# Kernel optimization log

Hardware: AMD Instinct MI355X
Metric: run time of the kernel (lower is better)

## Reference

```python
import jax, jax.numpy as jnp
import numpy as np

B, NPTS, NBOX = 16, 100000, 64
PTS_THRESHOLD = 2048          # topk voxels kept per scene
GT_THRESHOLD = 2.5            # distance multiplier
VOXEL_SIZE = 0.01
TENSOR_STRIDE = 8             # stride of the level being pruned
SIZE = TENSOR_STRIDE * VOXEL_SIZE  # 0.08, per-voxel cell size at this level


def setup_inputs() -> dict:
    key = jax.random.key(0)
    k1, k2, k3 = jax.random.split(key, 3)
    scores = jax.random.normal(k1, (B, NPTS), dtype=jnp.float32)
    points = jax.random.uniform(k2, (B, NPTS, 3), dtype=jnp.float32)
    gt_centers = jax.random.uniform(k3, (B, NBOX, 3), dtype=jnp.float32)
    return {"scores": scores, "points": points, "gt_centers": gt_centers}


def reference(scores, points, gt_centers):
    # --- per-batch topk score mask (MEFPN3D._get_score_mask) ---
    _, idx = jax.lax.top_k(scores, PTS_THRESHOLD)          # [B, K]
    score_mask = jnp.zeros(scores.shape, dtype=bool)
    score_mask = score_mask.at[jnp.arange(B)[:, None], idx].set(True)  # scatter True

    # --- gt distance mask (MEFPN3D._get_gt_mask) ---
    # distances: [B, Npts, n_boxes]
    diff = points[:, :, None, :] - gt_centers[:, None, :, :]
    distances = jnp.sqrt(jnp.sum(diff * diff, axis=-1))
    gt_mask = jnp.any(distances < SIZE * GT_THRESHOLD, axis=-1)        # [B, Npts]

    # --- combined prune mask (scatter of per-batch masks into global mask) ---
    prune_mask = jnp.logical_or(score_mask, gt_mask)

    # --- per-voxel sigmoid BCE loss, reduction='none' (CrossEntropyLoss use_sigmoid=True) ---
    target = gt_mask.astype(scores.dtype)
    losses = target * jax.nn.softplus(-scores) + (1.0 - target) * jax.nn.softplus(scores)
    return prune_mask, losses
```

## Files before the change

kernel.cpp:

```cpp
#include <hip/hip_runtime.h>
#include <hip/hip_bf16.h>
#include <stdint.h>

#define BB 16
#define NPTS 100000
#define NBOX 64
#define KTOP 2048
#define THRF 0.2f
#define C_LO 0.039984f
#define C_HI 0.040016f

#define SLICES 16
#define SLICE_SPAN 6272
#define SCAP 512
#define LIST_CAP 4096
#define CUT 0xC0000000u

#define CAND_OFF 0
#define CNT_OFF  (BB * SLICES * SCAP)
#define STATE_OFF (CNT_OFF + BB * SLICES)
#define TBOX_OFF  (STATE_OFF + BB * 2)

__device__ __forceinline__ uint32_t fmap(float f) {
    uint32_t b = __float_as_uint(f);
    return (b & 0x80000000u) ? ~b : (b | 0x80000000u);
}

__global__ __launch_bounds__(256) void cand_k(const float* __restrict__ scores,
                                              uint32_t* __restrict__ ws) {
    __shared__ uint32_t buf[SCAP];
    __shared__ uint32_t lcnt;
    const int b = blockIdx.y, sl = blockIdx.x, tid = threadIdx.x;
    if (tid == 0) lcnt = 0;
    __syncthreads();
    const int start = sl * SLICE_SPAN;
    const int nf4 = min(SLICE_SPAN, NPTS - start) >> 2;
    const float4* sc4 = reinterpret_cast<const float4*>(scores + (size_t)b * NPTS + start);
    for (int i4 = tid; i4 < nf4; i4 += 256) {
        const float4 v = sc4[i4];
        const uint32_t u[4] = {fmap(v.x), fmap(v.y), fmap(v.z), fmap(v.w)};
#pragma unroll
        for (int j = 0; j < 4; ++j) {
            if (u[j] >= CUT) {
                const uint32_t pos = atomicAdd(&lcnt, 1u);
                if (pos < SCAP) buf[pos] = u[j];
            }
        }
    }
    __syncthreads();
    const uint32_t c = lcnt;
    uint32_t* dst = ws + CAND_OFF + ((size_t)(b * SLICES + sl)) * SCAP;
    const uint32_t cw = c < SCAP ? c : SCAP;
    for (uint32_t i = tid; i < cw; i += 256) dst[i] = buf[i];
    if (tid == 0) ws[CNT_OFF + b * SLICES + sl] = c;
}

__device__ __forceinline__ void pick256(const uint32_t* __restrict__ hist,
                                        uint32_t* __restrict__ excl,
                                        int tid, int lane, uint32_t target,
                                        uint32_t* sBin, uint32_t* sKrem,
                                        uint32_t* sE, uint32_t* sTot, int wantE) {
    __syncthreads();
    if (tid < 64) {
        const uint32_t v0 = hist[4*tid], v1 = hist[4*tid+1], v2 = hist[4*tid+2], v3 = hist[4*tid+3];
        const uint32_t lt = v0 + v1 + v2 + v3;
        uint32_t x = lt;
#pragma unroll
        for (int off = 1; off < 64; off <<= 1) {
            const uint32_t y = __shfl_up(x, off);
            if (lane >= off) x += y;
        }
        const uint32_t ex = x - lt;
        excl[4*tid] = ex; excl[4*tid+1] = ex + v0;
        excl[4*tid+2] = ex + v0 + v1; excl[4*tid+3] = ex + v0 + v1 + v2;
        if (tid == 63) *sTot = x;
    }
    __syncthreads();
    {
        const uint32_t total = *sTot, lim = total - target;
        const uint32_t pe = excl[tid];
        const uint32_t pe1 = (tid == 255) ? total : excl[tid + 1];
        if (pe <= lim && pe1 > lim) {
            *sBin = (uint32_t)tid;
            *sKrem = target - (total - pe1);
            if (wantE) *sE = pe1 - pe;
        }
    }
    __syncthreads();
}

__global__ __launch_bounds__(256) void selfin_k(const float* __restrict__ scores,
                                                const float* __restrict__ ctrs,
                                                uint32_t* __restrict__ ws) {
    const int b = blockIdx.x, tid = threadIdx.x, w = tid >> 6, lane = tid & 63;
    __shared__ uint32_t list[LIST_CAP];
    __shared__ uint32_t h4[4][257];
    __shared__ uint32_t hist[256], excl[256];
    __shared__ uint32_t scnt[SLICES], soff[SLICES];
    __shared__ uint32_t wcnt[4];
    __shared__ uint32_t sBin, sKrem, sE, sTot, sIstar, sRun, sSpec, sUni, lcnt;

    const float* sc = scores + (size_t)b * NPTS;

    if (tid < NBOX) {
        const float cx = ctrs[(size_t)b * NBOX * 3 + 3 * tid];
        const float cy = ctrs[(size_t)b * NBOX * 3 + 3 * tid + 1];
        const float cz = ctrs[(size_t)b * NBOX * 3 + 3 * tid + 2];
        float4* TB = reinterpret_cast<float4*>(ws + TBOX_OFF) + b * NBOX;
        TB[tid] = make_float4(-2.0f * cx, -2.0f * cy, -2.0f * cz,
                              fmaf(cx, cx, fmaf(cy, cy, cz * cz)));
    }

    if (tid < SLICES) scnt[tid] = ws[CNT_OFF + b * SLICES + tid];
    __syncthreads();
    if (tid == 0) {
        uint32_t tot = 0; bool ok = true;
        for (int s = 0; s < SLICES; ++s) {
            soff[s] = tot;
            const uint32_t c = scnt[s];
            if (c > SCAP) ok = false;
            tot += c;
        }
        sTot = tot;
        sSpec = (ok && tot >= KTOP && tot <= LIST_CAP) ? 1u : 0u;
        sKrem = KTOP;
        sIstar = NPTS;
        lcnt = 0;
        sUni = 1u;
    }
    __syncthreads();

    uint32_t cnt, prefix = 0u;
    int shift0;
    if (sSpec) {
        cnt = sTot;
#pragma unroll 2
        for (int s = 0; s < SLICES; ++s) {
            const uint32_t c = scnt[s], o = soff[s];
            const uint32_t* src = ws + CAND_OFF + ((size_t)(b * SLICES + s)) * SCAP;
            for (uint32_t i = tid; i < c; i += 256) list[o + i] = src[i];
        }
        __syncthreads();
        const uint32_t b0 = list[0] >> 24;
        bool uni = true;
        for (uint32_t i = tid; i < cnt; i += 256) uni &= ((list[i] >> 24) == b0);
        if (!uni) atomicAnd(&sUni, 0u);
        __syncthreads();
        if (sUni) { prefix = b0 << 24; shift0 = 16; }
        else      { prefix = 0u;       shift0 = 24; }
    } else {
        for (int i = tid; i < 4 * 257; i += 256) (&h4[0][0])[i] = 0;
        __syncthreads();
        const float4* sc4 = reinterpret_cast<const float4*>(sc);
        for (int i4 = tid; i4 < NPTS / 4; i4 += 256) {
            const float4 v = sc4[i4];
            atomicAdd(&h4[w][fmap(v.x) >> 24], 1u);
            atomicAdd(&h4[w][fmap(v.y) >> 24], 1u);
            atomicAdd(&h4[w][fmap(v.z) >> 24], 1u);
            atomicAdd(&h4[w][fmap(v.w) >> 24], 1u);
        }
        __syncthreads();
        hist[tid] = h4[0][tid] + h4[1][tid] + h4[2][tid] + h4[3][tid];
        pick256(hist, excl, tid, lane, KTOP, &sBin, &sKrem, &sE, &sTot, 0);
        const uint32_t beta = sBin;
        for (int i4 = tid; i4 < NPTS / 4; i4 += 256) {
            const float4 v = sc4[i4];
            const uint32_t u[4] = {fmap(v.x), fmap(v.y), fmap(v.z), fmap(v.w)};
#pragma unroll
            for (int j = 0; j < 4; ++j) {
                if ((u[j] >> 24) == beta) {
                    const uint32_t pos = atomicAdd(&lcnt, 1u);
                    if (pos < LIST_CAP) list[pos] = u[j];
                }
            }
        }
        __syncthreads();
        cnt = lcnt < LIST_CAP ? lcnt : LIST_CAP;
        prefix = beta << 24;
        shift0 = 16;
    }

#pragma unroll 1
    for (int shift = shift0; shift >= 0; shift -= 8) {
        for (int i = tid; i < 4 * 257; i += 256) (&h4[0][0])[i] = 0;
        __syncthreads();
        const uint32_t hi8 = (shift < 24) ? (prefix >> (shift + 8)) : 0u;
        uint32_t* mh = h4[lane & 3];
        for (uint32_t i = tid; i < cnt; i += 256) {
            const uint32_t uu = list[i];
            const bool m = (shift == 24) || ((uu >> (shift + 8)) == hi8);
            if (m) atomicAdd(&mh[(uu >> shift) & 255u], 1u);
        }
        __syncthreads();
        hist[tid] = h4[0][tid] + h4[1][tid] + h4[2][tid] + h4[3][tid];
        const uint32_t target = sKrem;
        pick256(hist, excl, tid, lane, target, &sBin, &sKrem, &sE, &sTot,
                shift == 0 ? 1 : 0);
        prefix |= sBin << shift;
    }

    const uint32_t R = sKrem, E = sE;
    const uint32_t tbits = (prefix & 0x80000000u) ? (prefix & 0x7fffffffu) : ~prefix;

    if (E != R) {
        const float T = __uint_as_float(tbits);
        if (tid == 0) sRun = 0;
        __syncthreads();
        for (int base = 0; base < NPTS; base += 256) {
            const uint32_t r0 = sRun;
            if (r0 > R) break;
            const int i = base + tid;
            const bool eq = (i < NPTS) && (sc[i] == T);
            const unsigned long long mask = __ballot(eq);
            if (lane == 0) wcnt[w] = (uint32_t)__popcll(mask);
            __syncthreads();
            uint32_t before = 0, total = 0;
#pragma unroll
            for (int ww = 0; ww < 4; ++ww) {
                const uint32_t c = wcnt[ww];
                if (ww < w) before += c;
                total += c;
            }
            if (eq) {
                const uint32_t rank = r0 + before +
                    (uint32_t)__popcll(mask & ((1ull << lane) - 1ull));
                if (rank == R) sIstar = (uint32_t)i;
            }
            __syncthreads();
            if (tid == 0) sRun = r0 + total;
            __syncthreads();
        }
        __syncthreads();
    }
    if (tid == 0) {
        uint32_t* st = ws + STATE_OFF + b * 2;
        st[0] = tbits;
        st[1] = sIstar;
    }
}

__device__ __noinline__ bool exact_gt(float px, float py, float pz,
                                      const float* __restrict__ C) {
    bool hit = false;
#pragma unroll 1
    for (int k = 0; k < NBOX; ++k) {
        float dx = px - C[3 * k + 0];
        float dy = py - C[3 * k + 1];
        float dz = pz - C[3 * k + 2];
        float d2 = __fadd_rn(__fadd_rn(__fmul_rn(dx, dx), __fmul_rn(dy, dy)),
                             __fmul_rn(dz, dz));
        if (__fsqrt_rn(d2) < THRF) hit = true;
    }
    return hit;
}

__global__ __launch_bounds__(256) void main_k(const float* __restrict__ scores,
                                              const float* __restrict__ points,
                                              const float* __restrict__ ctrs,
                                              const uint32_t* __restrict__ ws,
                                              float* __restrict__ out) {
    const int b = blockIdx.y;
    const int i = blockIdx.x * 256 + threadIdx.x;
    if (i >= NPTS) return;

    const uint32_t* st = ws + STATE_OFF + b * 2;
    const float T = __uint_as_float(st[0]);
    const uint32_t Istar = st[1];
    const float4* __restrict__ TB =
        reinterpret_cast<const float4*>(ws + TBOX_OFF) + b * NBOX;

    const float* P = points + ((size_t)b * NPTS + i) * 3;
    const float px = P[0], py = P[1], pz = P[2];
    float m2 = 1e30f;

#pragma unroll
    for (int k = 0; k < NBOX; ++k) {
        const float4 B = TB[k];
        const float t = fmaf(B.x, px, fmaf(B.y, py, fmaf(B.z, pz, B.w)));
        m2 = fminf(m2, t);
    }

    const float s = scores[(size_t)b * NPTS + i];
    const float pp = fmaf(px, px, fmaf(py, py, pz * pz));
    const float m = pp + m2;
    bool gt;
    if (m < C_LO) gt = true;
    else if (m >= C_HI) gt = false;
    else gt = exact_gt(px, py, pz, ctrs + b * NBOX * 3);
    const bool sm = (s > T) || (s == T && (uint32_t)i < Istar);
    const float x = gt ? -s : s;
    const float ls = fmaxf(x, 0.0f) + __logf(1.0f + __expf(-fabsf(s)));
    out[(size_t)b * NPTS + i] = (gt || sm) ? 1.0f : 0.0f;
    out[(size_t)BB * NPTS + (size_t)b * NPTS + i] = ls;
}

extern "C" void kernel_launch(void* const* d_in, const int* in_sizes, int n_in,
                              void* d_out, int out_size, void* d_ws, size_t ws_size,
                              hipStream_t stream) {
    const float* scores = (const float*)d_in[0];
    const float* points = (const float*)d_in[1];
    const float* ctrs   = (const float*)d_in[2];
    float* out = (float*)d_out;
    uint32_t* ws = (uint32_t*)d_ws;

    const dim3 gridC(SLICES, BB);
    cand_k<<<gridC, 256, 0, stream>>>(scores, ws);
    selfin_k<<<BB, 256, 0, stream>>>(scores, ctrs, ws);
    const dim3 gridP((NPTS + 255) / 256, BB);
    main_k<<<gridP, 256, 0, stream>>>(scores, points, ctrs, ws, out);
}
```

Measured before the change: 47.70 us.

## Build box table in LDS per block, flatten candidate gather, nontemporal stores

The precomputed box table moves out of the selection kernel's global workspace. Each main-kernel block now builds it in shared memory and reads it from LDS instead of from global memory. The candidate gather in the selection kernel becomes one flat loop that finds each element's slice by binary search, replacing the per-slice loops. The main kernel's outputs use nontemporal stores and its box loop unroll drops to 8, at the cost of an extra barrier and redundant per-block table setup.

New measurement: 68.13 us. +42.8%, slower.

```diff
diff --git a/kernel.cpp b/kernel.cpp
--- a/kernel.cpp
+++ b/kernel.cpp
@@ -19,7 +19,6 @@
 #define CAND_OFF 0
 #define CNT_OFF  (BB * SLICES * SCAP)
 #define STATE_OFF (CNT_OFF + BB * SLICES)
-#define TBOX_OFF  (STATE_OFF + BB * 2)
 
 __device__ __forceinline__ uint32_t fmap(float f) {
     uint32_t b = __float_as_uint(f);
@@ -96,21 +95,10 @@
     __shared__ uint32_t list[LIST_CAP];
     __shared__ uint32_t h4[4][257];
     __shared__ uint32_t hist[256], excl[256];
-    __shared__ uint32_t scnt[SLICES], soff[SLICES];
+    __shared__ uint32_t scnt[SLICES], soff[SLICES + 1];
     __shared__ uint32_t wcnt[4];
     __shared__ uint32_t sBin, sKrem, sE, sTot, sIstar, sRun, sSpec, sUni, lcnt;
-
     const float* sc = scores + (size_t)b * NPTS;
-
-    if (tid < NBOX) {
-        const float cx = ctrs[(size_t)b * NBOX * 3 + 3 * tid];
-        const float cy = ctrs[(size_t)b * NBOX * 3 + 3 * tid + 1];
-        const float cz = ctrs[(size_t)b * NBOX * 3 + 3 * tid + 2];
-        float4* TB = reinterpret_cast<float4*>(ws + TBOX_OFF) + b * NBOX;
-        TB[tid] = make_float4(-2.0f * cx, -2.0f * cy, -2.0f * cz,
-                              fmaf(cx, cx, fmaf(cy, cy, cz * cz)));
-    }
-
     if (tid < SLICES) scnt[tid] = ws[CNT_OFF + b * SLICES + tid];
     __syncthreads();
     if (tid == 0) {
@@ -121,24 +109,23 @@
             if (c > SCAP) ok = false;
             tot += c;
         }
+        soff[SLICES] = tot;
         sTot = tot;
         sSpec = (ok && tot >= KTOP && tot <= LIST_CAP) ? 1u : 0u;
-        sKrem = KTOP;
-        sIstar = NPTS;
-        lcnt = 0;
-        sUni = 1u;
-    }
-    __syncthreads();
-
+        sKrem = KTOP; sIstar = NPTS; lcnt = 0; sUni = 1u;
+    }
+    __syncthreads();
     uint32_t cnt, prefix = 0u;
     int shift0;
     if (sSpec) {
         cnt = sTot;
-#pragma unroll 2
-        for (int s = 0; s < SLICES; ++s) {
-            const uint32_t c = scnt[s], o = soff[s];
-            const uint32_t* src = ws + CAND_OFF + ((size_t)(b * SLICES + s)) * SCAP;
-            for (uint32_t i = tid; i < c; i += 256) list[o + i] = src[i];
+        for (uint32_t i = tid; i < cnt; i += 256) {
+            int lo = 0, hi = SLICES - 1;
+            while (lo < hi) {
+                const int mid = (lo + hi + 1) >> 1;
+                if (soff[mid] <= i) lo = mid; else hi = mid - 1;
+            }
+            list[i] = ws[CAND_OFF + ((size_t)(b * SLICES + lo)) * SCAP + (i - soff[lo])];
         }
         __syncthreads();
         const uint32_t b0 = list[0] >> 24;
@@ -176,10 +163,8 @@
         }
         __syncthreads();
         cnt = lcnt < LIST_CAP ? lcnt : LIST_CAP;
-        prefix = beta << 24;
-        shift0 = 16;
-    }
-
+        prefix = beta << 24; shift0 = 16;
+    }
 #pragma unroll 1
     for (int shift = shift0; shift >= 0; shift -= 8) {
         for (int i = tid; i < 4 * 257; i += 256) (&h4[0][0])[i] = 0;
@@ -194,14 +179,11 @@
         __syncthreads();
         hist[tid] = h4[0][tid] + h4[1][tid] + h4[2][tid] + h4[3][tid];
         const uint32_t target = sKrem;
-        pick256(hist, excl, tid, lane, target, &sBin, &sKrem, &sE, &sTot,
-                shift == 0 ? 1 : 0);
+        pick256(hist, excl, tid, lane, target, &sBin, &sKrem, &sE, &sTot, shift == 0 ? 1 : 0);
         prefix |= sBin << shift;
     }
-
     const uint32_t R = sKrem, E = sE;
     const uint32_t tbits = (prefix & 0x80000000u) ? (prefix & 0x7fffffffu) : ~prefix;
-
     if (E != R) {
         const float T = __uint_as_float(tbits);
         if (tid == 0) sRun = 0;
@@ -222,8 +204,7 @@
                 total += c;
             }
             if (eq) {
-                const uint32_t rank = r0 + before +
-                    (uint32_t)__popcll(mask & ((1ull << lane) - 1ull));
+                const uint32_t rank = r0 + before + (uint32_t)__popcll(mask & ((1ull << lane) - 1ull));
                 if (rank == R) sIstar = (uint32_t)i;
             }
             __syncthreads();
@@ -233,9 +214,8 @@
         __syncthreads();
     }
     if (tid == 0) {
-        uint32_t* st = ws + STATE_OFF + b * 2;
-        st[0] = tbits;
-        st[1] = sIstar;
+        ws[STATE_OFF + b * 2] = tbits;
+        ws[STATE_OFF + b * 2 + 1] = sIstar;
     }
 }
 
@@ -259,23 +239,28 @@
                                               const float* __restrict__ ctrs,
                                               const uint32_t* __restrict__ ws,
                                               float* __restrict__ out) {
-    const int b = blockIdx.y;
-    const int i = blockIdx.x * 256 + threadIdx.x;
+    __shared__ float4 sbox[NBOX];
+    const int b = blockIdx.y, tid = threadIdx.x;
+    const float* __restrict__ C = ctrs + (size_t)b * NBOX * 3;
+    if (tid < NBOX) {
+        const float cx = C[3 * tid], cy = C[3 * tid + 1], cz = C[3 * tid + 2];
+        sbox[tid] = make_float4(-2.0f * cx, -2.0f * cy, -2.0f * cz,
+                                fmaf(cx, cx, fmaf(cy, cy, cz * cz)));
+    }
+    __syncthreads();
+
+    const int i = blockIdx.x * 256 + tid;
     if (i >= NPTS) return;
 
-    const uint32_t* st = ws + STATE_OFF + b * 2;
-    const float T = __uint_as_float(st[0]);
-    const uint32_t Istar = st[1];
-    const float4* __restrict__ TB =
-        reinterpret_cast<const float4*>(ws + TBOX_OFF) + b * NBOX;
+    const float T = __uint_as_float(ws[STATE_OFF + b * 2]);
+    const uint32_t Istar = ws[STATE_OFF + b * 2 + 1];
 
     const float* P = points + ((size_t)b * NPTS + i) * 3;
     const float px = P[0], py = P[1], pz = P[2];
     float m2 = 1e30f;
-
-#pragma unroll
+#pragma unroll 8
     for (int k = 0; k < NBOX; ++k) {
-        const float4 B = TB[k];
+        const float4 B = sbox[k];
         const float t = fmaf(B.x, px, fmaf(B.y, py, fmaf(B.z, pz, B.w)));
         m2 = fminf(m2, t);
     }
@@ -286,12 +271,12 @@
     bool gt;
     if (m < C_LO) gt = true;
     else if (m >= C_HI) gt = false;
-    else gt = exact_gt(px, py, pz, ctrs + b * NBOX * 3);
+    else gt = exact_gt(px, py, pz, C);
     const bool sm = (s > T) || (s == T && (uint32_t)i < Istar);
     const float x = gt ? -s : s;
     const float ls = fmaxf(x, 0.0f) + __logf(1.0f + __expf(-fabsf(s)));
-    out[(size_t)b * NPTS + i] = (gt || sm) ? 1.0f : 0.0f;
-    out[(size_t)BB * NPTS + (size_t)b * NPTS + i] = ls;
+    __builtin_nontemporal_store((gt || sm) ? 1.0f : 0.0f, out + (size_t)b * NPTS + i);
+    __builtin_nontemporal_store(ls, out + (size_t)BB * NPTS + (size_t)b * NPTS + i);
 }
 
 extern "C" void kernel_launch(void* const* d_in, const int* in_sizes, int n_in,
```
